# Optimization experiments

Hardware: AMD Instinct MI355X
Metric: run time of the kernel (lower is better)

Reference implementation:

```python
import jax, jax.numpy as jnp
import numpy as np

IMG, P, C, E = 256, 16, 3, 200
N = (IMG // P) ** 2          # 256 patches
NUM_MASKED = int(N * 0.75)   # 192
PATCH_ELEMS = C * P * P      # 768


def setup_inputs() -> dict:
    key = jax.random.key(0)
    ks = jax.random.split(key, 10)
    B = 128
    x = jax.random.normal(ks[0], (B, C, IMG, IMG), dtype=jnp.float32)
    perm = jax.random.permutation(ks[1], N).astype(jnp.int32)
    conv_w = jax.random.normal(ks[2], (E, C, P, P), dtype=jnp.float32) * 0.02
    conv_b = jnp.zeros((E,), dtype=jnp.float32)
    pos_embed = jax.random.normal(ks[3], (1, N, E), dtype=jnp.float32) * 0.02
    mask_token = jnp.zeros((1, E), dtype=jnp.float32)
    W_enc = jax.random.normal(ks[4], (E, E), dtype=jnp.float32) * (1.0 / np.sqrt(E))
    b_enc = jnp.zeros((E,), dtype=jnp.float32)
    W_dec = jax.random.normal(ks[5], (E, PATCH_ELEMS), dtype=jnp.float32) * (1.0 / np.sqrt(E))
    b_dec = jnp.zeros((PATCH_ELEMS,), dtype=jnp.float32)
    return {"x": x, "conv_w": conv_w, "conv_b": conv_b, "pos_embed": pos_embed,
            "mask_token": mask_token, "W_enc": W_enc, "b_enc": b_enc,
            "W_dec": W_dec, "b_dec": b_dec, "perm": perm}


def _patchify(x):
    # [B,C,H,W] -> [B, N, C*P*P], row-major patch order (matches conv stride=P then flatten)
    B = x.shape[0]
    g = IMG // P
    x = x.reshape(B, C, g, P, g, P)           # B C gh P gw P
    x = x.transpose(0, 2, 4, 1, 3, 5)         # B gh gw C P P
    return x.reshape(B, g * g, C * P * P)


def _fold(patches):
    # [B, N, C*P*P] -> [B,C,H,W]; idx iterates rows (i) outer, cols (j) inner
    B = patches.shape[0]
    g = IMG // P
    p = patches.reshape(B, g, g, C, P, P)
    return p.transpose(0, 3, 1, 4, 2, 5).reshape(B, C, IMG, IMG)


def reference(x, conv_w, conv_b, pos_embed, mask_token, W_enc, b_enc, W_dec, b_dec, perm):
    masked_idx = perm[:NUM_MASKED]
    unmasked_idx = perm[NUM_MASKED:]
    # patch embed (Conv2d k=P, stride=P == linear over flattened patches)
    patches = _patchify(x)                                   # [B,N,768]
    w_flat = conv_w.reshape(E, -1)                           # [E, 768]
    emb = jnp.einsum('bnp,ep->bne', patches, w_flat) + conv_b + pos_embed  # [B,N,E]
    visible = emb[:, unmasked_idx, :]                        # [B, N-192, E]
    encoded = jnp.einsum('bne,ef->bnf', visible, W_enc) + b_enc
    B = x.shape[0]
    full = jnp.zeros((B, N, E), dtype=x.dtype)
    full = full.at[:, unmasked_idx, :].set(encoded)
    full = full.at[:, masked_idx, :].set(jnp.broadcast_to(mask_token, (B, NUM_MASKED, E)))
    full = full + pos_embed
    dec = jnp.einsum('bne,ep->bnp', full, W_dec) + b_dec     # [B,N,768]
    img = _fold(dec)                                         # [B,C,H,W]
    return img, masked_idx
```

## Files before the change

kernel.cpp:

```cpp
#include <hip/hip_runtime.h>

typedef __attribute__((ext_vector_type(8))) __bf16 bf16x8;
typedef __attribute__((ext_vector_type(4))) float f32x4;

constexpr int Bsz   = 128;
constexpr int EE    = 200;
constexpr int EP    = 256;
constexpr int KP    = 224;
constexpr int NN    = 256;
constexpr int NMASK = 192;
constexpr int NVIS  = 64;
constexpr int PE    = 768;
constexpr int M1    = Bsz * NVIS;
constexpr int M3    = M1 + NMASK;
constexpr long IMG_ELEMS = (long)Bsz * 3 * 256 * 256;

__global__ __launch_bounds__(256) void k_prep(
    const float* __restrict__ pos, const float* __restrict__ wflat,
    const float* __restrict__ Wenc, const float* __restrict__ Wdec,
    const float* __restrict__ conv_b, const float* __restrict__ b_enc,
    const float* __restrict__ mask_token, const int* __restrict__ perm,
    float* __restrict__ posP, __bf16* __restrict__ W1t,
    __bf16* __restrict__ W2t, __bf16* __restrict__ W3t,
    float* __restrict__ cbp, float* __restrict__ bep,
    __bf16* __restrict__ full, float* __restrict__ out_idx)
{
    int blk = blockIdx.x, t = threadIdx.x;
    if (blk < 256) {
        posP[blk * 256 + t] = (t < EE) ? pos[blk * EE + t] : 0.f;
        return;
    }
    blk -= 256;
    if (blk < 768) {
        int e = blk / 3, k = (blk % 3) * 256 + t;
        W1t[e * 768 + k] = (e < EE) ? (__bf16)wflat[e * 768 + k] : (__bf16)0.f;
        return;
    }
    blk -= 768;
    if (blk < 256) {
        if (t < KP) W2t[blk * KP + t] =
            (blk < EE && t < EE) ? (__bf16)Wenc[t * EE + blk] : (__bf16)0.f;
        return;
    }
    blk -= 256;
    if (blk < 768) {
        if (t < KP) W3t[blk * KP + t] =
            (t < EE) ? (__bf16)Wdec[t * PE + blk] : (__bf16)0.f;
        return;
    }
    blk -= 768;
    if (blk < NMASK) {
        int n = perm[blk];
        full[(M1 + blk) * EP + t] =
            (t < EE) ? (__bf16)(mask_token[t] + pos[n * EE + t]) : (__bf16)0.f;
        return;
    }
    cbp[t] = (t < EE) ? conv_b[t] : 0.f;
    bep[t] = (t < EE) ? b_enc[t] : 0.f;
    if (t < NMASK) out_idx[t] = (float)perm[t];
}

__global__ __launch_bounds__(256) void k_gemm1(
    const float* __restrict__ x, const __bf16* __restrict__ W1t,
    const float* __restrict__ cbp, const float* __restrict__ posP,
    const int* __restrict__ perm, __bf16* __restrict__ visible)
{
    __shared__ __bf16 As[64][40];
    __shared__ __bf16 Bs[64][40];
    const int t = threadIdx.x;
    const int m0 = blockIdx.y * 64, e0 = blockIdx.x * 64;
    const int row = t >> 2, chunk = t & 3;
    const int lane = t & 63, wid = t >> 6;
    const int wr = wid >> 1, wc = wid & 1;
    const int quad = lane >> 4, lid = lane & 15;

    const int am = m0 + row;
    const int an = perm[NMASK + (am & 63)];
    const int abase = (am >> 6) * 196608 + (an >> 4) * 4096 + (an & 15) * 16;

    f32x4 acc[2][2] = {};

    for (int k0 = 0; k0 < PE; k0 += 32) {
        int k = k0 + chunk * 8;
        int c = k >> 8, py = (k >> 4) & 15, px = k & 15;
        const float* ap = x + abase + c * 65536 + py * 256 + px;
        float4 a0 = *(const float4*)ap;
        float4 a1 = *(const float4*)(ap + 4);
        bf16x8 av;
        av[0] = (__bf16)a0.x; av[1] = (__bf16)a0.y; av[2] = (__bf16)a0.z; av[3] = (__bf16)a0.w;
        av[4] = (__bf16)a1.x; av[5] = (__bf16)a1.y; av[6] = (__bf16)a1.z; av[7] = (__bf16)a1.w;
        *(bf16x8*)&As[row][chunk * 8] = av;
        *(int4*)&Bs[row][chunk * 8] = *(const int4*)&W1t[(e0 + row) * 768 + k];
        __syncthreads();
        #pragma unroll
        for (int i = 0; i < 2; ++i) {
            bf16x8 af = *(const bf16x8*)&As[wr * 32 + i * 16 + lid][quad * 8];
            #pragma unroll
            for (int j = 0; j < 2; ++j) {
                bf16x8 bfv = *(const bf16x8*)&Bs[wc * 32 + j * 16 + lid][quad * 8];
                acc[i][j] = __builtin_amdgcn_mfma_f32_16x16x32_bf16(af, bfv, acc[i][j], 0, 0, 0);
            }
        }
        __syncthreads();
    }

    #pragma unroll
    for (int i = 0; i < 2; ++i) {
        int mb = m0 + wr * 32 + i * 16 + quad * 4;
        #pragma unroll
        for (int j = 0; j < 2; ++j) {
            int e = e0 + wc * 32 + j * 16 + lid;
            #pragma unroll
            for (int r = 0; r < 4; ++r) {
                int m = mb + r;
                int n = perm[NMASK + (m & 63)];
                float v = acc[i][j][r] + cbp[e] + posP[n * 256 + e];
                visible[m * EP + e] = (__bf16)v;
            }
        }
    }
}

__global__ __launch_bounds__(256) void k_gemm2(
    const __bf16* __restrict__ visible, const __bf16* __restrict__ W2t,
    const float* __restrict__ bep, const float* __restrict__ posP,
    const int* __restrict__ perm, __bf16* __restrict__ full)
{
    __shared__ __bf16 As[64][40];
    __shared__ __bf16 Bs[64][40];
    const int t = threadIdx.x;
    const int m0 = blockIdx.y * 64, e0 = blockIdx.x * 64;
    const int row = t >> 2, chunk = t & 3;
    const int lane = t & 63, wid = t >> 6;
    const int wr = wid >> 1, wc = wid & 1;
    const int quad = lane >> 4, lid = lane & 15;

    f32x4 acc[2][2] = {};

    for (int k0 = 0; k0 < KP; k0 += 32) {
        int k = k0 + chunk * 8;
        *(int4*)&As[row][chunk * 8] = *(const int4*)&visible[(m0 + row) * EP + k];
        *(int4*)&Bs[row][chunk * 8] = *(const int4*)&W2t[(e0 + row) * KP + k];
        __syncthreads();
        #pragma unroll
        for (int i = 0; i < 2; ++i) {
            bf16x8 af = *(const bf16x8*)&As[wr * 32 + i * 16 + lid][quad * 8];
            #pragma unroll
            for (int j = 0; j < 2; ++j) {
                bf16x8 bfv = *(const bf16x8*)&Bs[wc * 32 + j * 16 + lid][quad * 8];
                acc[i][j] = __builtin_amdgcn_mfma_f32_16x16x32_bf16(af, bfv, acc[i][j], 0, 0, 0);
            }
        }
        __syncthreads();
    }

    #pragma unroll
    for (int i = 0; i < 2; ++i) {
        int mb = m0 + wr * 32 + i * 16 + quad * 4;
        #pragma unroll
        for (int j = 0; j < 2; ++j) {
            int e = e0 + wc * 32 + j * 16 + lid;
            #pragma unroll
            for (int r = 0; r < 4; ++r) {
                int m = mb + r;
                int n = perm[NMASK + (m & 63)];
                float v = acc[i][j][r] + bep[e] + posP[n * 256 + e];
                full[m * EP + e] = (__bf16)v;
            }
        }
    }
}

__global__ __launch_bounds__(256) void k_gemm3(
    const __bf16* __restrict__ full, const __bf16* __restrict__ W3t,
    const float* __restrict__ bdec, const int* __restrict__ perm,
    float* __restrict__ img, float* __restrict__ dec_masked)
{
    __shared__ __bf16 As[64][40];
    __shared__ __bf16 Bs[64][40];
    const int t = threadIdx.x;
    const int m0 = blockIdx.y * 64, e0 = blockIdx.x * 64;
    const int row = t >> 2, chunk = t & 3;
    const int lane = t & 63, wid = t >> 6;
    const int wr = wid >> 1, wc = wid & 1;
    const int quad = lane >> 4, lid = lane & 15;

    f32x4 acc[2][2] = {};

    for (int k0 = 0; k0 < KP; k0 += 32) {
        int k = k0 + chunk * 8;
        *(int4*)&As[row][chunk * 8] = *(const int4*)&full[(m0 + row) * EP + k];
        *(int4*)&Bs[row][chunk * 8] = *(const int4*)&W3t[(e0 + row) * KP + k];
        __syncthreads();
        #pragma unroll
        for (int i = 0; i < 2; ++i) {
            bf16x8 af = *(const bf16x8*)&As[wr * 32 + i * 16 + lid][quad * 8];
            #pragma unroll
            for (int j = 0; j < 2; ++j) {
                bf16x8 bfv = *(const bf16x8*)&Bs[wc * 32 + j * 16 + lid][quad * 8];
                acc[i][j] = __builtin_amdgcn_mfma_f32_16x16x32_bf16(af, bfv, acc[i][j], 0, 0, 0);
            }
        }
        __syncthreads();
    }

    const bool vis = (m0 < M1);
    #pragma unroll
    for (int i = 0; i < 2; ++i) {
        int mb = m0 + wr * 32 + i * 16 + quad * 4;
        #pragma unroll
        for (int j = 0; j < 2; ++j) {
            int e = e0 + wc * 32 + j * 16 + lid;
            int c = e >> 8, py = (e >> 4) & 15, px = e & 15;
            #pragma unroll
            for (int r = 0; r < 4; ++r) {
                int m = mb + r;
                float v = acc[i][j][r] + bdec[e];
                if (vis) {
                    int b = m >> 6;
                    int n = perm[NMASK + (m & 63)];
                    img[(long)(b * 3 + c) * 65536 + ((n >> 4) * 16 + py) * 256
                        + (n & 15) * 16 + px] = v;
                } else {
                    dec_masked[(m - M1) * PE + e] = v;
                }
            }
        }
    }
}

__global__ __launch_bounds__(192) void k_foldmask(
    const float* __restrict__ dec_masked, const int* __restrict__ perm,
    float* __restrict__ img)
{
    const int i = blockIdx.x;
    const int b = blockIdx.y;
    const int n = perm[i];
    const int t = threadIdx.x;
    float4 v = *(const float4*)&dec_masked[i * PE + t * 4];
    int p = t * 4;
    int c = p >> 8, py = (p >> 4) & 15, px = p & 15;
    *(float4*)&img[(long)(b * 3 + c) * 65536 + ((n >> 4) * 16 + py) * 256
                   + (n & 15) * 16 + px] = v;
}

extern "C" void kernel_launch(void* const* d_in, const int* in_sizes, int n_in,
                              void* d_out, int out_size, void* d_ws, size_t ws_size,
                              hipStream_t stream)
{
    const float* x          = (const float*)d_in[0];
    const float* conv_w     = (const float*)d_in[1];
    const float* conv_b     = (const float*)d_in[2];
    const float* pos        = (const float*)d_in[3];
    const float* mask_token = (const float*)d_in[4];
    const float* W_enc      = (const float*)d_in[5];
    const float* b_enc      = (const float*)d_in[6];
    const float* W_dec      = (const float*)d_in[7];
    const float* b_dec      = (const float*)d_in[8];
    const int*   perm       = (const int*)d_in[9];
    float* out = (float*)d_out;

    __bf16* visible = (__bf16*)d_ws;
    __bf16* full    = visible + M1 * EP;
    __bf16* W1t     = full + M3 * EP;
    __bf16* W2t     = W1t + 256 * 768;
    __bf16* W3t     = W2t + 256 * KP;
    float*  posP    = (float*)(W3t + 768 * KP);
    float*  cbp     = posP + 256 * 256;
    float*  bep     = cbp + 256;
    float*  decm    = bep + 256;

    k_prep<<<256 + 768 + 256 + 768 + NMASK + 1, 256, 0, stream>>>(
        pos, conv_w, W_enc, W_dec, conv_b, b_enc, mask_token, perm,
        posP, W1t, W2t, W3t, cbp, bep, full, out + IMG_ELEMS);
    k_gemm1<<<dim3(4, 128), 256, 0, stream>>>(x, W1t, cbp, posP, perm, visible);
    k_gemm2<<<dim3(4, 128), 256, 0, stream>>>(visible, W2t, bep, posP, perm, full);
    k_gemm3<<<dim3(12, 131), 256, 0, stream>>>(full, W3t, b_dec, perm, out, decm);
    k_foldmask<<<dim3(NMASK, Bsz), 192, 0, stream>>>(decm, perm, out);
}
```

Before: 243.4 us.

## Fuse encoder GEMMs via LDS staging and enlarge decoder tiles with direct loads

The patch-embed GEMM and the encoder GEMM are merged into one kernel, k_enc. Each block computes 32 visible rows across all 256 features, keeps the intermediate in LDS, and then runs the second GEMM from there, which removes the global 'visible' buffer and one launch. The decoder GEMM moves to 128x128 tiles with 4x4 MFMA fragments per wave. It loads operands straight from global memory with no LDS staging or barriers. In exchange, k_enc runs only 256 blocks, decoder operand reuse now relies on cache, and each thread holds more registers.

```diff
diff --git a/kernel.cpp b/kernel.cpp
--- a/kernel.cpp
+++ b/kernel.cpp
@@ -7,7 +7,6 @@
 constexpr int EE    = 200;
 constexpr int EP    = 256;
 constexpr int KP    = 224;
-constexpr int NN    = 256;
 constexpr int NMASK = 192;
 constexpr int NVIS  = 64;
 constexpr int PE    = 768;
@@ -60,168 +59,157 @@
     if (t < NMASK) out_idx[t] = (float)perm[t];
 }
 
-__global__ __launch_bounds__(256) void k_gemm1(
+__global__ __launch_bounds__(256) void k_enc(
     const float* __restrict__ x, const __bf16* __restrict__ W1t,
-    const float* __restrict__ cbp, const float* __restrict__ posP,
-    const int* __restrict__ perm, __bf16* __restrict__ visible)
-{
-    __shared__ __bf16 As[64][40];
-    __shared__ __bf16 Bs[64][40];
-    const int t = threadIdx.x;
-    const int m0 = blockIdx.y * 64, e0 = blockIdx.x * 64;
-    const int row = t >> 2, chunk = t & 3;
-    const int lane = t & 63, wid = t >> 6;
-    const int wr = wid >> 1, wc = wid & 1;
-    const int quad = lane >> 4, lid = lane & 15;
-
-    const int am = m0 + row;
-    const int an = perm[NMASK + (am & 63)];
-    const int abase = (am >> 6) * 196608 + (an >> 4) * 4096 + (an & 15) * 16;
-
-    f32x4 acc[2][2] = {};
-
-    for (int k0 = 0; k0 < PE; k0 += 32) {
-        int k = k0 + chunk * 8;
-        int c = k >> 8, py = (k >> 4) & 15, px = k & 15;
-        const float* ap = x + abase + c * 65536 + py * 256 + px;
-        float4 a0 = *(const float4*)ap;
-        float4 a1 = *(const float4*)(ap + 4);
-        bf16x8 av;
-        av[0] = (__bf16)a0.x; av[1] = (__bf16)a0.y; av[2] = (__bf16)a0.z; av[3] = (__bf16)a0.w;
-        av[4] = (__bf16)a1.x; av[5] = (__bf16)a1.y; av[6] = (__bf16)a1.z; av[7] = (__bf16)a1.w;
-        *(bf16x8*)&As[row][chunk * 8] = av;
-        *(int4*)&Bs[row][chunk * 8] = *(const int4*)&W1t[(e0 + row) * 768 + k];
-        __syncthreads();
-        #pragma unroll
-        for (int i = 0; i < 2; ++i) {
-            bf16x8 af = *(const bf16x8*)&As[wr * 32 + i * 16 + lid][quad * 8];
-            #pragma unroll
-            for (int j = 0; j < 2; ++j) {
-                bf16x8 bfv = *(const bf16x8*)&Bs[wc * 32 + j * 16 + lid][quad * 8];
-                acc[i][j] = __builtin_amdgcn_mfma_f32_16x16x32_bf16(af, bfv, acc[i][j], 0, 0, 0);
-            }
-        }
-        __syncthreads();
-    }
-
-    #pragma unroll
-    for (int i = 0; i < 2; ++i) {
-        int mb = m0 + wr * 32 + i * 16 + quad * 4;
-        #pragma unroll
-        for (int j = 0; j < 2; ++j) {
-            int e = e0 + wc * 32 + j * 16 + lid;
-            #pragma unroll
-            for (int r = 0; r < 4; ++r) {
-                int m = mb + r;
-                int n = perm[NMASK + (m & 63)];
-                float v = acc[i][j][r] + cbp[e] + posP[n * 256 + e];
-                visible[m * EP + e] = (__bf16)v;
-            }
-        }
-    }
-}
-
-__global__ __launch_bounds__(256) void k_gemm2(
-    const __bf16* __restrict__ visible, const __bf16* __restrict__ W2t,
+    const __bf16* __restrict__ W2t, const float* __restrict__ cbp,
     const float* __restrict__ bep, const float* __restrict__ posP,
     const int* __restrict__ perm, __bf16* __restrict__ full)
 {
-    __shared__ __bf16 As[64][40];
-    __shared__ __bf16 Bs[64][40];
+    __shared__ __bf16 visLds[32][264];
     const int t = threadIdx.x;
-    const int m0 = blockIdx.y * 64, e0 = blockIdx.x * 64;
-    const int row = t >> 2, chunk = t & 3;
-    const int lane = t & 63, wid = t >> 6;
-    const int wr = wid >> 1, wc = wid & 1;
+    const int w = t >> 6;
+    const int lane = t & 63;
     const int quad = lane >> 4, lid = lane & 15;
-
-    f32x4 acc[2][2] = {};
-
+    const int m0 = blockIdx.x * 32;
+
+    int abase[2], nrow[2];
+    #pragma unroll
+    for (int i = 0; i < 2; ++i) {
+        int m = m0 + i * 16 + lid;
+        int n = perm[NMASK + (m & 63)];
+        nrow[i] = n;
+        abase[i] = (m >> 6) * 196608 + (n >> 4) * 4096 + (n & 15) * 16;
+    }
+
+    f32x4 acc[2][4] = {};
+    for (int k0 = 0; k0 < PE; k0 += 32) {
+        int k = k0 + quad * 8;
+        int c = k >> 8, py = (k >> 4) & 15, px = k & 15;
+        int aoff = c * 65536 + py * 256 + px;
+        bf16x8 af[2];
+        #pragma unroll
+        for (int i = 0; i < 2; ++i) {
+            const float* ap = x + abase[i] + aoff;
+            float4 a0 = *(const float4*)ap;
+            float4 a1 = *(const float4*)(ap + 4);
+            af[i][0] = (__bf16)a0.x; af[i][1] = (__bf16)a0.y;
+            af[i][2] = (__bf16)a0.z; af[i][3] = (__bf16)a0.w;
+            af[i][4] = (__bf16)a1.x; af[i][5] = (__bf16)a1.y;
+            af[i][6] = (__bf16)a1.z; af[i][7] = (__bf16)a1.w;
+        }
+        #pragma unroll
+        for (int j = 0; j < 4; ++j) {
+            int f = w * 64 + j * 16 + lid;
+            bf16x8 bv = *(const bf16x8*)&W1t[f * 768 + k];
+            acc[0][j] = __builtin_amdgcn_mfma_f32_16x16x32_bf16(af[0], bv, acc[0][j], 0, 0, 0);
+            acc[1][j] = __builtin_amdgcn_mfma_f32_16x16x32_bf16(af[1], bv, acc[1][j], 0, 0, 0);
+        }
+    }
+
+    #pragma unroll
+    for (int i = 0; i < 2; ++i) {
+        #pragma unroll
+        for (int j = 0; j < 4; ++j) {
+            int f = w * 64 + j * 16 + lid;
+            float bias = cbp[f];
+            #pragma unroll
+            for (int r = 0; r < 4; ++r) {
+                int lm = i * 16 + quad * 4 + r;
+                int n = perm[NMASK + ((m0 + lm) & 63)];
+                visLds[lm][f] = (__bf16)(acc[i][j][r] + bias + posP[n * 256 + f]);
+            }
+        }
+    }
+    __syncthreads();
+
+    f32x4 acc2[2][4] = {};
     for (int k0 = 0; k0 < KP; k0 += 32) {
-        int k = k0 + chunk * 8;
-        *(int4*)&As[row][chunk * 8] = *(const int4*)&visible[(m0 + row) * EP + k];
-        *(int4*)&Bs[row][chunk * 8] = *(const int4*)&W2t[(e0 + row) * KP + k];
-        __syncthreads();
-        #pragma unroll
-        for (int i = 0; i < 2; ++i) {
-            bf16x8 af = *(const bf16x8*)&As[wr * 32 + i * 16 + lid][quad * 8];
-            #pragma unroll
-            for (int j = 0; j < 2; ++j) {
-                bf16x8 bfv = *(const bf16x8*)&Bs[wc * 32 + j * 16 + lid][quad * 8];
-                acc[i][j] = __builtin_amdgcn_mfma_f32_16x16x32_bf16(af, bfv, acc[i][j], 0, 0, 0);
+        int k = k0 + quad * 8;
+        bf16x8 av[2];
+        #pragma unroll
+        for (int i = 0; i < 2; ++i)
+            av[i] = *(const bf16x8*)&visLds[i * 16 + lid][k];
+        #pragma unroll
+        for (int j = 0; j < 4; ++j) {
+            int f = w * 64 + j * 16 + lid;
+            bf16x8 bv = *(const bf16x8*)&W2t[f * KP + k];
+            acc2[0][j] = __builtin_amdgcn_mfma_f32_16x16x32_bf16(av[0], bv, acc2[0][j], 0, 0, 0);
+            acc2[1][j] = __builtin_amdgcn_mfma_f32_16x16x32_bf16(av[1], bv, acc2[1][j], 0, 0, 0);
+        }
+    }
+
+    #pragma unroll
+    for (int i = 0; i < 2; ++i) {
+        #pragma unroll
+        for (int j = 0; j < 4; ++j) {
+            int f = w * 64 + j * 16 + lid;
+            float bias = bep[f];
+            #pragma unroll
+            for (int r = 0; r < 4; ++r) {
+                int lm = i * 16 + quad * 4 + r;
+                int m = m0 + lm;
+                int n = perm[NMASK + (m & 63)];
+                full[m * EP + f] = (__bf16)(acc2[i][j][r] + bias + posP[n * 256 + f]);
             }
         }
-        __syncthreads();
-    }
-
-    #pragma unroll
-    for (int i = 0; i < 2; ++i) {
-        int mb = m0 + wr * 32 + i * 16 + quad * 4;
-        #pragma unroll
-        for (int j = 0; j < 2; ++j) {
-            int e = e0 + wc * 32 + j * 16 + lid;
-            #pragma unroll
-            for (int r = 0; r < 4; ++r) {
-                int m = mb + r;
-                int n = perm[NMASK + (m & 63)];
-                float v = acc[i][j][r] + bep[e] + posP[n * 256 + e];
-                full[m * EP + e] = (__bf16)v;
-            }
-        }
-    }
-}
-
-__global__ __launch_bounds__(256) void k_gemm3(
+    }
+}
+
+__global__ __launch_bounds__(256) void k_dec(
     const __bf16* __restrict__ full, const __bf16* __restrict__ W3t,
     const float* __restrict__ bdec, const int* __restrict__ perm,
     float* __restrict__ img, float* __restrict__ dec_masked)
 {
-    __shared__ __bf16 As[64][40];
-    __shared__ __bf16 Bs[64][40];
     const int t = threadIdx.x;
-    const int m0 = blockIdx.y * 64, e0 = blockIdx.x * 64;
-    const int row = t >> 2, chunk = t & 3;
-    const int lane = t & 63, wid = t >> 6;
-    const int wr = wid >> 1, wc = wid & 1;
+    const int w = t >> 6, lane = t & 63;
+    const int wr = w >> 1, wc = w & 1;
     const int quad = lane >> 4, lid = lane & 15;
-
-    f32x4 acc[2][2] = {};
-
+    const int m0 = blockIdx.y * 128, e0 = blockIdx.x * 128;
+
+    int mrow[4];
+    #pragma unroll
+    for (int i = 0; i < 4; ++i) {
+        int m = m0 + wr * 64 + i * 16 + lid;
+        mrow[i] = (m < M3) ? m : (M3 - 1);
+    }
+
+    f32x4 acc[4][4] = {};
     for (int k0 = 0; k0 < KP; k0 += 32) {
-        int k = k0 + chunk * 8;
-        *(int4*)&As[row][chunk * 8] = *(const int4*)&full[(m0 + row) * EP + k];
-        *(int4*)&Bs[row][chunk * 8] = *(const int4*)&W3t[(e0 + row) * KP + k];
-        __syncthreads();
-        #pragma unroll
-        for (int i = 0; i < 2; ++i) {
-            bf16x8 af = *(const bf16x8*)&As[wr * 32 + i * 16 + lid][quad * 8];
-            #pragma unroll
-            for (int j = 0; j < 2; ++j) {
-                bf16x8 bfv = *(const bf16x8*)&Bs[wc * 32 + j * 16 + lid][quad * 8];
-                acc[i][j] = __builtin_amdgcn_mfma_f32_16x16x32_bf16(af, bfv, acc[i][j], 0, 0, 0);
-            }
-        }
-        __syncthreads();
-    }
-
-    const bool vis = (m0 < M1);
-    #pragma unroll
-    for (int i = 0; i < 2; ++i) {
-        int mb = m0 + wr * 32 + i * 16 + quad * 4;
-        #pragma unroll
-        for (int j = 0; j < 2; ++j) {
-            int e = e0 + wc * 32 + j * 16 + lid;
+        int k = k0 + quad * 8;
+        bf16x8 av[4], bv[4];
+        #pragma unroll
+        for (int i = 0; i < 4; ++i)
+            av[i] = *(const bf16x8*)&full[mrow[i] * EP + k];
+        #pragma unroll
+        for (int j = 0; j < 4; ++j) {
+            int f = e0 + wc * 64 + j * 16 + lid;
+            bv[j] = *(const bf16x8*)&W3t[f * KP + k];
+        }
+        #pragma unroll
+        for (int i = 0; i < 4; ++i)
+            #pragma unroll
+            for (int j = 0; j < 4; ++j)
+                acc[i][j] = __builtin_amdgcn_mfma_f32_16x16x32_bf16(av[i], bv[j], acc[i][j], 0, 0, 0);
+    }
+
+    #pragma unroll
+    for (int i = 0; i < 4; ++i) {
+        int mb = m0 + wr * 64 + i * 16 + quad * 4;
+        #pragma unroll
+        for (int j = 0; j < 4; ++j) {
+            int e = e0 + wc * 64 + j * 16 + lid;
             int c = e >> 8, py = (e >> 4) & 15, px = e & 15;
+            float bias = bdec[e];
             #pragma unroll
             for (int r = 0; r < 4; ++r) {
                 int m = mb + r;
-                float v = acc[i][j][r] + bdec[e];
-                if (vis) {
+                float v = acc[i][j][r] + bias;
+                if (m < M1) {
                     int b = m >> 6;
                     int n = perm[NMASK + (m & 63)];
                     img[(long)(b * 3 + c) * 65536 + ((n >> 4) * 16 + py) * 256
                         + (n & 15) * 16 + px] = v;
-                } else {
+                } else if (m < M3) {
                     dec_masked[(m - M1) * PE + e] = v;
                 }
             }
@@ -260,21 +248,19 @@
     const int*   perm       = (const int*)d_in[9];
     float* out = (float*)d_out;
 
-    __bf16* visible = (__bf16*)d_ws;
-    __bf16* full    = visible + M1 * EP;
-    __bf16* W1t     = full + M3 * EP;
-    __bf16* W2t     = W1t + 256 * 768;
-    __bf16* W3t     = W2t + 256 * KP;
-    float*  posP    = (float*)(W3t + 768 * KP);
-    float*  cbp     = posP + 256 * 256;
-    float*  bep     = cbp + 256;
-    float*  decm    = bep + 256;
+    __bf16* full = (__bf16*)d_ws;
+    __bf16* W1t  = full + M3 * EP;
+    __bf16* W2t  = W1t + 256 * 768;
+    __bf16* W3t  = W2t + 256 * KP;
+    float*  posP = (float*)(W3t + 768 * KP);
+    float*  cbp  = posP + 256 * 256;
+    float*  bep  = cbp + 256;
+    float*  decm = bep + 256;
 
     k_prep<<<256 + 768 + 256 + 768 + NMASK + 1, 256, 0, stream>>>(
         pos, conv_w, W_enc, W_dec, conv_b, b_enc, mask_token, perm,
         posP, W1t, W2t, W3t, cbp, bep, full, out + IMG_ELEMS);
-    k_gemm1<<<dim3(4, 128), 256, 0, stream>>>(x, W1t, cbp, posP, perm, visible);
-    k_gemm2<<<dim3(4, 128), 256, 0, stream>>>(visible, W2t, bep, posP, perm, full);
-    k_gemm3<<<dim3(12, 131), 256, 0, stream>>>(full, W3t, b_dec, perm, out, decm);
+    k_enc<<<256, 256, 0, stream>>>(x, W1t, W2t, cbp, bep, posP, perm, full);
+    k_dec<<<dim3(6, 66), 256, 0, stream>>>(full, W3t, b_dec, perm, out, decm);
     k_foldmask<<<dim3(NMASK, Bsz), 192, 0, stream>>>(decm, perm, out);
 }
```

Result: no change. 244.0 us (+0.3%).
